# Kernel optimization log

Measured on AMD Instinct MI355X. Metric: run time of the kernel, lower is better.

The kernel has to match this reference:

```python
import jax, jax.numpy as jnp
import numpy as np

B, T, H, W = 512, 8, 28, 28
VTH, VRESET = 1.0, 0.0
ALPHA = 2.0  # spikingjelly ATan surrogate default alpha


@jax.custom_vjp
def heaviside_atan(x):
    # forward: binary spike; backward: ATan surrogate gradient
    return (x >= 0).astype(x.dtype)

def _ha_fwd(x):
    return (x >= 0).astype(x.dtype), x

def _ha_bwd(x, g):
    return (g * (ALPHA / 2.0) / (1.0 + (jnp.pi / 2.0 * ALPHA * x) ** 2),)

heaviside_atan.defvjp(_ha_fwd, _ha_bwd)


def conv3x3(x, w):
    return jax.lax.conv_general_dilated(
        x, w, (1, 1), 'SAME', dimension_numbers=('NCHW', 'OIHW', 'NCHW'))


def maxpool2(x):
    return jax.lax.reduce_window(x, -jnp.inf, jax.lax.max,
                                 (1, 1, 2, 2), (1, 1, 2, 2), 'VALID')


def one_spike_if(v, fired, x):
    # OneSpikeIFNode: integrate, fire at most once (fired mask), hard reset
    v = v + x
    spike = heaviside_atan(v - VTH) * (1.0 - fired)
    v = v * (1.0 - spike) + VRESET * spike
    fired = jnp.maximum(fired, jax.lax.stop_gradient(spike))
    return v, fired, spike


def if_node(v, x):
    # readout IFNode: integrate, fire, hard reset (v_threshold finite: latency mode, no warmup)
    v = v + x
    spike = heaviside_atan(v - VTH)
    v = v * (1.0 - spike) + VRESET * spike
    return v, spike


def setup_inputs() -> dict:
    key = jax.random.key(0)
    k = jax.random.split(key, 5)
    x = jax.random.uniform(k[0], (B, 1, H, W), jnp.float32)
    # weight scale (default_T / T) == 1 since T == 8 == default_T
    w_sconv = jax.random.normal(k[1], (16, 1, 3, 3), jnp.float32) * (2.0 / 3.0)
    w_conv = jax.random.normal(k[2], (16, 16, 3, 3), jnp.float32) * 0.12
    w_fc1 = jax.random.normal(k[3], (100, 16 * 14 * 14), jnp.float32) * 0.02
    w_fc2 = jax.random.normal(k[4], (10, 100), jnp.float32) * 0.15
    return {"x": x, "w_sconv": w_sconv, "w_conv": w_conv, "w_fc1": w_fc1, "w_fc2": w_fc2}


def reference(x, w_sconv, w_conv, w_fc1, w_fc2):
    xs = conv3x3(x, w_sconv)  # static conv computed once, reused every timestep
    z = jnp.zeros_like(xs)                       # [B,16,28,28]
    zp = jnp.zeros((B, 16, 14, 14), xs.dtype)    # pool fired-window mask
    zf = jnp.zeros((B, 100), xs.dtype)
    zo = jnp.zeros((B, 10), xs.dtype)
    state0 = (z, z, z, z, zp, zf, zf, zo)

    def step(state, _):
        v1, f1, v2, f2, pf, vfc, ffc, vout = state
        v1, f1, s1 = one_spike_if(v1, f1, xs)
        c = conv3x3(s1, w_conv)
        v2, f2, s2 = one_spike_if(v2, f2, c)
        # FirstSpikePool2d: max-pool spikes, each window passes only its first spike
        pooled = maxpool2(s2) * (1.0 - pf)
        pf = jnp.maximum(pf, jax.lax.stop_gradient(pooled))
        h = pooled.reshape(B, -1) @ w_fc1.T      # [B,100]
        vfc, ffc, s3 = one_spike_if(vfc, ffc, h)
        o = s3 @ w_fc2.T                          # [B,10]
        vout, s4 = if_node(vout, o)
        fr = jnp.stack([s1.mean(), s2.mean(), s3.mean(), s4.mean()])
        return (v1, f1, v2, f2, pf, vfc, ffc, vout), (s4, vout, fr)

    _, (s4_t, vout_t, fr_t) = jax.lax.scan(step, state0, None, length=T)
    counter_t = jnp.cumsum(s4_t, axis=0)                        # [T,B,10]
    latency_score = heaviside_atan(counter_t - 0.5).sum(axis=0)  # ATan_binary surrogate
    reg_loss = fr_t.max(axis=0).sum()
    return latency_score / T, reg_loss
```

## Files before the change

### kernel.cpp

```cpp
#include <hip/hip_runtime.h>

#define TB 1024
#define NIMG 512
#define HW 28
#define NPIX 784
#define TT 8
#define NFC 100
#define NOUT 10
#define MAGIC 0x5C5C5C5Cu

#define WT_FLOATS 313600
#define GLB_ADD(p, v) __hip_atomic_fetch_add((p), (v), __ATOMIC_RELAXED, __HIP_MEMORY_SCOPE_AGENT)

typedef float f4 __attribute__((ext_vector_type(4)));

__device__ __forceinline__ void wave_sum4(unsigned int& a, unsigned int& b,
                                          unsigned int& c, unsigned int& d) {
#pragma unroll
    for (int s = 1; s < 64; s <<= 1) {
        a += __shfl_xor(a, s);
        b += __shfl_xor(b, s);
        c += __shfl_xor(c, s);
        d += __shfl_xor(d, s);
    }
}

__global__ __launch_bounds__(TB, 8)
void snn_main(const float* __restrict__ xg, const float* __restrict__ w_sconv,
              const float* __restrict__ w_conv, const float* __restrict__ w_fc1,
              const float* __restrict__ w_fc2, float* __restrict__ wT,
              float* __restrict__ out, unsigned int* __restrict__ ctrl)
{
    __shared__ float wc[2880];
    __shared__ unsigned char spanB[25600];
    __shared__ unsigned short rowOr[TT * HW];
    __shared__ unsigned char tqA[3136];
    __shared__ unsigned short slist[3136];
    __shared__ float xst[NPIX];
    __shared__ float wsc[144];
    __shared__ int bcnt[9], bofs[9], bput[8];
    __shared__ int hist[32];
    __shared__ int lastflag;

    unsigned short* mask_t = (unsigned short*)spanB;
    unsigned int* mask32 = (unsigned int*)spanB;
    unsigned int* t2n = (unsigned int*)(spanB + 12544);
    float* prefixLDS = (float*)spanB;

    unsigned int* tflags = ctrl;
    float* fr_g = (float*)(ctrl + 98);
    unsigned int* done2 = ctrl + 130;
    unsigned int* fr_ready = ctrl + 131;

    const int tid = threadIdx.x;
    const int b = blockIdx.x;
    const int lane = tid & 63;

    if (b < 98) {
        const int c0 = b * 32;
        for (int idx = tid; idx < 3200; idx += TB) {
            int c = idx / 100, r = idx - 100 * c;
            wT[(c0 + c) * 100 + r] = w_fc1[r * 3136 + c0 + c];
        }
    }
    if (b == 0 && tid < 33) ctrl[98 + tid] = 0u;

    for (int i = tid; i < NPIX; i += TB) xst[i] = xg[b * NPIX + i];
    for (int i = tid; i < 144; i += TB) wsc[i] = w_sconv[i];
    for (int i = tid; i < 2304; i += TB) {
        int c = i & 15, r = i >> 4;
        wc[r * 20 + c] = w_conv[c * 144 + r];
    }
    for (int i = tid; i < 3136; i += TB) mask32[i] = 0u;
    if (tid < 32) hist[tid] = 0;
    if (tid < 9) bcnt[tid] = 0;
    if (b < 98) __threadfence();
    __syncthreads();
    if (b < 98 && tid == 0) {
        __hip_atomic_store(&tflags[b], MAGIC, __ATOMIC_RELEASE, __HIP_MEMORY_SCOPE_AGENT);
        if (b == 0)
            __hip_atomic_store(fr_ready, MAGIC, __ATOMIC_RELEASE, __HIP_MEMORY_SCOPE_AGENT);
    }

    unsigned int pca = 0, pcb = 0;
#pragma unroll 1
    for (int e = 0; e < 13; e++) {
        int g = e * TB + tid;
        if (g < 12544) {
            int ci = g & 15, pos = g >> 4;
            int yy = pos / HW, xx = pos % HW;
            float acc = 0.f;
#pragma unroll
            for (int ky = 0; ky < 3; ky++) {
                int ys = yy + ky - 1;
                if (ys < 0 || ys >= HW) continue;
#pragma unroll
                for (int kx = 0; kx < 3; kx++) {
                    int xsrc = xx + kx - 1;
                    if (xsrc < 0 || xsrc >= HW) continue;
                    acc = fmaf(wsc[ci * 9 + ky * 3 + kx], xst[ys * HW + xsrc], acc);
                }
            }
            int t1 = 8; float v = 0.f;
#pragma unroll
            for (int t = 0; t < TT; t++) {
                v += acc;
                if (t1 == 8 && v >= 1.0f) t1 = t;
            }
            if (t1 < 8) {
                int lin = t1 * NPIX + pos;
                atomicOr(&mask32[lin >> 1], (1u << ci) << ((lin & 1) * 16));
                if (t1 < 4) pca += 1u << (t1 * 8); else pcb += 1u << ((t1 - 4) * 8);
            }
        }
    }
    {
        unsigned int a_lo = pca & 0x00ff00ffu, a_hi = (pca >> 8) & 0x00ff00ffu;
        unsigned int b_lo = pcb & 0x00ff00ffu, b_hi = (pcb >> 8) & 0x00ff00ffu;
        wave_sum4(a_lo, a_hi, b_lo, b_hi);
        if (lane == 0) {
            if (a_lo & 0xffffu)  atomicAdd(&hist[0], (int)(a_lo & 0xffffu));
            if (a_hi & 0xffffu)  atomicAdd(&hist[1], (int)(a_hi & 0xffffu));
            if (a_lo >> 16)      atomicAdd(&hist[2], (int)(a_lo >> 16));
            if (a_hi >> 16)      atomicAdd(&hist[3], (int)(a_hi >> 16));
            if (b_lo & 0xffffu)  atomicAdd(&hist[4], (int)(b_lo & 0xffffu));
            if (b_hi & 0xffffu)  atomicAdd(&hist[5], (int)(b_hi & 0xffffu));
            if (b_lo >> 16)      atomicAdd(&hist[6], (int)(b_lo >> 16));
            if (b_hi >> 16)      atomicAdd(&hist[7], (int)(b_hi >> 16));
        }
    }
    __syncthreads();

    for (int i = tid; i < TT * HW; i += TB) {
        const unsigned short* mr = mask_t + (i / HW) * NPIX + (i % HW) * HW;
        unsigned int o = 0;
#pragma unroll
        for (int x = 0; x < HW; x++) o |= mr[x];
        rowOr[i] = (unsigned short)o;
    }
    __syncthreads();

    unsigned int pc2a = 0, pc2b = 0;
    {
        int run = tid >> 4;
        int pos = (run < 49) ? ((run * 18) % 49) * 16 + (tid & 15) : -1;
        if (pos >= 0) {
            int py = pos / HW, px = pos - py * HW;
            f4 vv0 = {0.f, 0.f, 0.f, 0.f}, vv1 = vv0, vv2 = vv0, vv3 = vv0;
            unsigned int done = 0;
            unsigned int t2lo = 0x88888888u, t2hi = 0x88888888u;
#pragma unroll 1
            for (int t = 0; t < TT; t++) {
                const unsigned short* ro = rowOr + t * HW;
                unsigned int un = ro[py];
                if (py > 0) un |= ro[py - 1];
                if (py < HW - 1) un |= ro[py + 1];
                if (!un) continue;
                const unsigned short* mt = mask_t + t * NPIX;
#pragma unroll
                for (int k = 0; k < 9; k++) {
                    int qy = py + k / 3 - 1, qx = px + k % 3 - 1;
                    if ((unsigned)qy >= HW || (unsigned)qx >= HW) continue;
                    unsigned int m = mt[qy * HW + qx];
                    while (m) {
                        int ci = __builtin_ctz(m); m &= m - 1;
                        const f4* wrow = (const f4*)&wc[(ci * 9 + k) * 20];
                        vv0 += wrow[0]; vv1 += wrow[1];
                        vv2 += wrow[2]; vv3 += wrow[3];
                    }
                }
                unsigned int fired = 0;
#pragma unroll
                for (int c = 0; c < 16; c++) {
                    float val = (c < 4) ? vv0[c & 3] : (c < 8) ? vv1[c & 3]
                              : (c < 12) ? vv2[c & 3] : vv3[c & 3];
                    fired |= (val >= 1.0f) ? (1u << c) : 0u;
                }
                unsigned int newf = fired & ~done;
                done |= newf;
                if (newf) {
                    int cnt = __builtin_popcount(newf);
                    if (t < 4) pc2a += (unsigned)cnt << (t * 8);
                    else       pc2b += (unsigned)cnt << ((t - 4) * 8);
                    while (newf) {
                        int c = __builtin_ctz(newf); newf &= newf - 1;
                        if (c < 8) t2lo = (t2lo & ~(15u << (4 * c))) | ((unsigned)t << (4 * c));
                        else       t2hi = (t2hi & ~(15u << (4 * (c - 8)))) | ((unsigned)t << (4 * (c - 8)));
                    }
                }
                if (done == 0xffffu) break;
            }
            t2n[pos * 2] = t2lo;
            t2n[pos * 2 + 1] = t2hi;
        }
    }
    {
        unsigned int a_lo = pc2a & 0x00ff00ffu, a_hi = (pc2a >> 8) & 0x00ff00ffu;
        unsigned int b_lo = pc2b & 0x00ff00ffu, b_hi = (pc2b >> 8) & 0x00ff00ffu;
        wave_sum4(a_lo, a_hi, b_lo, b_hi);
        if (lane == 0) {
            if (a_lo & 0xffffu)  atomicAdd(&hist[8],  (int)(a_lo & 0xffffu));
            if (a_hi & 0xffffu)  atomicAdd(&hist[9],  (int)(a_hi & 0xffffu));
            if (a_lo >> 16)      atomicAdd(&hist[10], (int)(a_lo >> 16));
            if (a_hi >> 16)      atomicAdd(&hist[11], (int)(a_hi >> 16));
            if (b_lo & 0xffffu)  atomicAdd(&hist[12], (int)(b_lo & 0xffffu));
            if (b_hi & 0xffffu)  atomicAdd(&hist[13], (int)(b_hi & 0xffffu));
            if (b_lo >> 16)      atomicAdd(&hist[14], (int)(b_lo >> 16));
            if (b_hi >> 16)      atomicAdd(&hist[15], (int)(b_hi >> 16));
        }
    }
    __syncthreads();

    {
        unsigned int cpa = 0, cpb = 0;
        for (int u = tid; u < 3136; u += TB) {
            int c = u / 196, rem = u - c * 196;
            int wy = rem / 14, wx = rem - wy * 14;
            int p0 = wy * 56 + wx * 2;
            int wsel = c >> 3, sh = (c & 7) * 4;
            int m0 = (t2n[p0 * 2 + wsel] >> sh) & 15;
            int m1 = (t2n[(p0 + 1) * 2 + wsel] >> sh) & 15;
            int m2 = (t2n[(p0 + HW) * 2 + wsel] >> sh) & 15;
            int m3 = (t2n[(p0 + HW + 1) * 2 + wsel] >> sh) & 15;
            int tqv = min(min(m0, m1), min(m2, m3));
            tqA[u] = (unsigned char)tqv;
            if (tqv < 8) {
                if (tqv < 4) cpa += 1u << (tqv * 8);
                else         cpb += 1u << ((tqv - 4) * 8);
            }
        }
        unsigned int a_lo = cpa & 0x00ff00ffu, a_hi = (cpa >> 8) & 0x00ff00ffu;
        unsigned int b_lo = cpb & 0x00ff00ffu, b_hi = (cpb >> 8) & 0x00ff00ffu;
        wave_sum4(a_lo, a_hi, b_lo, b_hi);
        if (lane == 0) {
            if (a_lo & 0xffffu)  atomicAdd(&bcnt[0], (int)(a_lo & 0xffffu));
            if (a_hi & 0xffffu)  atomicAdd(&bcnt[1], (int)(a_hi & 0xffffu));
            if (a_lo >> 16)      atomicAdd(&bcnt[2], (int)(a_lo >> 16));
            if (a_hi >> 16)      atomicAdd(&bcnt[3], (int)(a_hi >> 16));
            if (b_lo & 0xffffu)  atomicAdd(&bcnt[4], (int)(b_lo & 0xffffu));
            if (b_hi & 0xffffu)  atomicAdd(&bcnt[5], (int)(b_hi & 0xffffu));
            if (b_lo >> 16)      atomicAdd(&bcnt[6], (int)(b_lo >> 16));
            if (b_hi >> 16)      atomicAdd(&bcnt[7], (int)(b_hi >> 16));
        }
    }
    __syncthreads();
    if (tid == 0) {
        int s = 0;
#pragma unroll
        for (int t = 0; t < TT; t++) { bofs[t] = s; s += bcnt[t]; }
        bofs[8] = s;
    }
    __syncthreads();
    if (tid < 8) bput[tid] = bofs[tid];
    __syncthreads();
    for (int base_u = 0; base_u < 3136; base_u += TB) {
        int u = base_u + tid;
        int tqv = (u < 3136) ? (int)tqA[u] : 8;
#pragma unroll 1
        for (int v = 0; v < TT; v++) {
            unsigned long long m = __ballot(tqv == v);
            if (!m) continue;
            int lead = __ffsll((unsigned long long)m) - 1;
            int bs = 0;
            if (lane == lead) bs = atomicAdd(&bput[v], __popcll(m));
            bs = __shfl(bs, lead);
            if (tqv == v) {
                int rank = __popcll(m & ((1ull << lane) - 1ull));
                slist[bs + rank] = (unsigned short)u;
            }
        }
    }

    if (tid < 98) {
        while (__hip_atomic_load(&tflags[tid], __ATOMIC_ACQUIRE,
                                 __HIP_MEMORY_SCOPE_AGENT) != MAGIC)
            __builtin_amdgcn_s_sleep(2);
    }
    __syncthreads();

    {
        const int w = tid >> 7;
        const int sub = (tid >> 6) & 1;
        const int col = sub * 64 + lane;
        const bool act = col < NFC;
        const float* wA = wT + col;
        float acc0 = 0.f;
#pragma unroll 1
        for (int t = 0; t < TT; t++) {
            const int lo = bofs[t];
            const int n = bofs[t + 1] - lo;
            int j = w;
            for (; j + 56 < n; j += 64) {
                int u0 = (int)slist[lo + j] * 100;
                int u1 = (int)slist[lo + j + 8] * 100;
                int u2 = (int)slist[lo + j + 16] * 100;
                int u3 = (int)slist[lo + j + 24] * 100;
                int u4 = (int)slist[lo + j + 32] * 100;
                int u5 = (int)slist[lo + j + 40] * 100;
                int u6 = (int)slist[lo + j + 48] * 100;
                int u7 = (int)slist[lo + j + 56] * 100;
                if (act) {
                    float a0 = wA[u0], a1 = wA[u1], a2 = wA[u2], a3 = wA[u3];
                    float a4 = wA[u4], a5 = wA[u5], a6 = wA[u6], a7 = wA[u7];
                    acc0 += a0; acc0 += a1; acc0 += a2; acc0 += a3;
                    acc0 += a4; acc0 += a5; acc0 += a6; acc0 += a7;
                }
            }
            for (; j + 24 < n; j += 32) {
                int u0 = (int)slist[lo + j] * 100;
                int u1 = (int)slist[lo + j + 8] * 100;
                int u2 = (int)slist[lo + j + 16] * 100;
                int u3 = (int)slist[lo + j + 24] * 100;
                if (act) {
                    float a0 = wA[u0], a1 = wA[u1], a2 = wA[u2], a3 = wA[u3];
                    acc0 += a0; acc0 += a1; acc0 += a2; acc0 += a3;
                }
            }
            for (; j < n; j += 8) {
                int u0 = (int)slist[lo + j] * 100;
                if (act) acc0 += wA[u0];
            }
            if (act) prefixLDS[(w * TT + t) * NFC + col] = acc0;
        }
    }
    __syncthreads();

    if (tid < NFC) {
        int t3 = 8;
#pragma unroll
        for (int t = 0; t < TT; t++) {
            float v = 0.f;
#pragma unroll
            for (int w = 0; w < 8; w++) v += prefixLDS[(w * TT + t) * NFC + tid];
            if (t3 == 8 && v >= 1.0f) t3 = t;
        }
        tqA[tid] = (unsigned char)t3;
        if (t3 < 8) atomicAdd(&hist[16 + t3], 1);
    }
    __syncthreads();

    if (tid < 640) {
        const int o = tid >> 6;
        float acc8[TT] = {0.f, 0.f, 0.f, 0.f, 0.f, 0.f, 0.f, 0.f};
        {
            float wv = w_fc2[o * NFC + lane];
            int tv = tqA[lane];
#pragma unroll
            for (int k = 0; k < TT; k++) acc8[k] += (tv == k) ? wv : 0.f;
        }
        if (lane < 36) {
            float wv = w_fc2[o * NFC + 64 + lane];
            int tv = tqA[64 + lane];
#pragma unroll
            for (int k = 0; k < TT; k++) acc8[k] += (tv == k) ? wv : 0.f;
        }
#pragma unroll
        for (int s = 1; s < 64; s <<= 1) {
#pragma unroll
            for (int k = 0; k < TT; k++) acc8[k] += __shfl_xor(acc8[k], s);
        }
        if (lane == 0) {
            float vout = 0.f; int cnt = 0; float lat = 0.f;
#pragma unroll
            for (int t = 0; t < TT; t++) {
                vout += acc8[t];
                if (vout >= 1.0f) { vout = 0.f; cnt++; atomicAdd(&hist[24 + t], 1); }
                if (cnt >= 1) lat += 1.f;
            }
            out[b * NOUT + o] = lat * 0.125f;
        }
    }
    __syncthreads();

    if (tid == 0) {
        while (__hip_atomic_load(fr_ready, __ATOMIC_ACQUIRE,
                                 __HIP_MEMORY_SCOPE_AGENT) != MAGIC)
            __builtin_amdgcn_s_sleep(2);
    }
    __syncthreads();
    if (tid < 32) {
        int h = hist[tid];
        if (h) GLB_ADD(&fr_g[(tid & 7) * 4 + (tid >> 3)], (float)h);
    }
    __syncthreads();

    if (tid == 0) {
        unsigned int old = __hip_atomic_fetch_add(done2, 1u, __ATOMIC_ACQ_REL,
                                                  __HIP_MEMORY_SCOPE_AGENT);
        lastflag = (old == (unsigned)(NIMG - 1));
    }
    __syncthreads();
    if (lastflag && tid == 0) {
        const float inv0 = 1.f / 6422528.f;
        const float inv2 = 1.f / 51200.f;
        const float inv3 = 1.f / 5120.f;
        const float invs[4] = { inv0, inv0, inv2, inv3 };
        float reg = 0.f;
        for (int l = 0; l < 4; l++) {
            float mx = -INFINITY;
            for (int t = 0; t < TT; t++) {
                float v = __hip_atomic_load(&fr_g[t * 4 + l], __ATOMIC_RELAXED,
                                            __HIP_MEMORY_SCOPE_AGENT);
                mx = fmaxf(mx, v * invs[l]);
            }
            reg += mx;
        }
        out[NIMG * NOUT] = reg;
    }
}

extern "C" void kernel_launch(void* const* d_in, const int* in_sizes, int n_in,
                              void* d_out, int out_size, void* d_ws, size_t ws_size,
                              hipStream_t stream) {
    const float* x       = (const float*)d_in[0];
    const float* w_sconv = (const float*)d_in[1];
    const float* w_conv  = (const float*)d_in[2];
    const float* w_fc1   = (const float*)d_in[3];
    const float* w_fc2   = (const float*)d_in[4];
    float* out = (float*)d_out;

    float* wT          = (float*)d_ws;
    unsigned int* ctrl = (unsigned int*)(wT + WT_FLOATS);

    snn_main<<<NIMG, TB, 0, stream>>>(x, w_sconv, w_conv, w_fc1, w_fc2, wT,
                                      out, ctrl);
}
```

Before: 173.5 us.

## Pad spike mask planes and sort conv2 pixels by neighbor spike load

Stores the layer-1 first-spike masks in zero-padded 30x30 planes, so the conv2 gather reads nine neighbor masks without bounds checks. It packs them into five words and walks the set bits in one combined loop. It also counts layer-1 spikes per pixel and bucket-sorts the 784 output pixels by their 3x3 neighborhood spike count, so lanes in a wave get similar amounts of work and diverge less. This replaces the rowOr skip test and the fixed permutation, at the cost of extra ballot/atomic sorting passes and more shared memory.

```diff
diff --git a/kernel.cpp b/kernel.cpp
--- a/kernel.cpp
+++ b/kernel.cpp
@@ -4,6 +4,8 @@
 #define NIMG 512
 #define HW 28
 #define NPIX 784
+#define PW 30
+#define PPLANE 900
 #define TT 8
 #define NFC 100
 #define NOUT 10
@@ -33,19 +35,22 @@
 {
     __shared__ float wc[2880];
     __shared__ unsigned char spanB[25600];
-    __shared__ unsigned short rowOr[TT * HW];
-    __shared__ unsigned char tqA[3136];
+    __shared__ int tqAi[784];
     __shared__ unsigned short slist[3136];
     __shared__ float xst[NPIX];
     __shared__ float wsc[144];
     __shared__ int bcnt[9], bofs[9], bput[8];
+    __shared__ int s32cnt[32], s32ofs[33], s32put[32];
     __shared__ int hist[32];
     __shared__ int lastflag;
 
-    unsigned short* mask_t = (unsigned short*)spanB;
-    unsigned int* mask32 = (unsigned int*)spanB;
-    unsigned int* t2n = (unsigned int*)(spanB + 12544);
+    unsigned short* maskP = (unsigned short*)spanB;
+    unsigned int* maskP32 = (unsigned int*)spanB;
+    unsigned int* t2n = (unsigned int*)(spanB + 14400);
     float* prefixLDS = (float*)spanB;
+    unsigned char* tqA = (unsigned char*)tqAi;
+    unsigned char* cntA = (unsigned char*)tqAi;
+    unsigned short* sorted2 = slist;
 
     unsigned int* tflags = ctrl;
     float* fr_g = (float*)(ctrl + 98);
@@ -71,8 +76,9 @@
         int c = i & 15, r = i >> 4;
         wc[r * 20 + c] = w_conv[c * 144 + r];
     }
-    for (int i = tid; i < 3136; i += TB) mask32[i] = 0u;
-    if (tid < 32) hist[tid] = 0;
+    for (int i = tid; i < 3600; i += TB) maskP32[i] = 0u;
+    if (tid < 225) tqAi[tid] = 0;
+    if (tid < 32) { hist[tid] = 0; s32cnt[tid] = 0; }
     if (tid < 9) bcnt[tid] = 0;
     if (b < 98) __threadfence();
     __syncthreads();
@@ -86,9 +92,11 @@
 #pragma unroll 1
     for (int e = 0; e < 13; e++) {
         int g = e * TB + tid;
+        int t1 = 8;
+        int yy = 0, xx = 0;
         if (g < 12544) {
             int ci = g & 15, pos = g >> 4;
-            int yy = pos / HW, xx = pos % HW;
+            yy = pos / HW; xx = pos - yy * HW;
             float acc = 0.f;
 #pragma unroll
             for (int ky = 0; ky < 3; ky++) {
@@ -101,17 +109,22 @@
                     acc = fmaf(wsc[ci * 9 + ky * 3 + kx], xst[ys * HW + xsrc], acc);
                 }
             }
-            int t1 = 8; float v = 0.f;
+            float v = 0.f;
 #pragma unroll
             for (int t = 0; t < TT; t++) {
                 v += acc;
                 if (t1 == 8 && v >= 1.0f) t1 = t;
             }
             if (t1 < 8) {
-                int lin = t1 * NPIX + pos;
-                atomicOr(&mask32[lin >> 1], (1u << ci) << ((lin & 1) * 16));
+                int lin = t1 * PPLANE + (yy + 1) * PW + (xx + 1);
+                atomicOr(&maskP32[lin >> 1], (1u << ci) << ((lin & 1) * 16));
                 if (t1 < 4) pca += 1u << (t1 * 8); else pcb += 1u << ((t1 - 4) * 8);
             }
+        }
+        unsigned long long bal = __ballot(g < 12544 && t1 < 8);
+        if (g < 12544 && (tid & 15) == 0) {
+            int cnt = (int)__popcll((bal >> (lane & 48)) & 0xFFFFull);
+            cntA[(yy + 1) * PW + (xx + 1)] = (unsigned char)cnt;
         }
     }
     {
@@ -131,40 +144,70 @@
     }
     __syncthreads();
 
-    for (int i = tid; i < TT * HW; i += TB) {
-        const unsigned short* mr = mask_t + (i / HW) * NPIX + (i % HW) * HW;
-        unsigned int o = 0;
-#pragma unroll
-        for (int x = 0; x < HW; x++) o |= mr[x];
-        rowOr[i] = (unsigned short)o;
+    int myb = 32;
+    if (tid < NPIX) {
+        int py = tid / HW, px = tid - py * HW;
+        const unsigned char* cb = cntA + py * PW + px;
+        int nb = cb[0] + cb[1] + cb[2] + cb[PW] + cb[PW + 1] + cb[PW + 2]
+               + cb[2 * PW] + cb[2 * PW + 1] + cb[2 * PW + 2];
+        myb = min(nb >> 2, 31);
+    }
+#pragma unroll 1
+    for (int v = 0; v < 32; v++) {
+        unsigned long long mm = __ballot(myb == v);
+        if (mm && lane == 0) atomicAdd(&s32cnt[v], (int)__popcll(mm));
+    }
+    __syncthreads();
+    if (tid == 0) {
+        int s = 0;
+#pragma unroll 1
+        for (int v = 0; v < 32; v++) { s32ofs[v] = s; s += s32cnt[v]; }
+        s32ofs[32] = s;
+    }
+    __syncthreads();
+    if (tid < 32) s32put[tid] = s32ofs[tid];
+    __syncthreads();
+#pragma unroll 1
+    for (int v = 0; v < 32; v++) {
+        unsigned long long mm = __ballot(myb == v);
+        if (!mm) continue;
+        int lead = __ffsll(mm) - 1;
+        int bs = 0;
+        if (lane == lead) bs = atomicAdd(&s32put[v], (int)__popcll(mm));
+        bs = __shfl(bs, lead);
+        if (myb == v) {
+            int rank = (int)__popcll(mm & ((1ull << lane) - 1ull));
+            sorted2[bs + rank] = (unsigned short)tid;
+        }
     }
     __syncthreads();
 
     unsigned int pc2a = 0, pc2b = 0;
     {
-        int run = tid >> 4;
-        int pos = (run < 49) ? ((run * 18) % 49) * 16 + (tid & 15) : -1;
+        const int pos = (tid < NPIX) ? (int)sorted2[tid] : -1;
         if (pos >= 0) {
-            int py = pos / HW, px = pos - py * HW;
+            const int py = pos / HW, px = pos - py * HW;
+            const unsigned short* mbase = maskP + py * PW + px;
             f4 vv0 = {0.f, 0.f, 0.f, 0.f}, vv1 = vv0, vv2 = vv0, vv3 = vv0;
             unsigned int done = 0;
             unsigned int t2lo = 0x88888888u, t2hi = 0x88888888u;
 #pragma unroll 1
             for (int t = 0; t < TT; t++) {
-                const unsigned short* ro = rowOr + t * HW;
-                unsigned int un = ro[py];
-                if (py > 0) un |= ro[py - 1];
-                if (py < HW - 1) un |= ro[py + 1];
-                if (!un) continue;
-                const unsigned short* mt = mask_t + t * NPIX;
-#pragma unroll
-                for (int k = 0; k < 9; k++) {
-                    int qy = py + k / 3 - 1, qx = px + k % 3 - 1;
-                    if ((unsigned)qy >= HW || (unsigned)qx >= HW) continue;
-                    unsigned int m = mt[qy * HW + qx];
-                    while (m) {
-                        int ci = __builtin_ctz(m); m &= m - 1;
-                        const f4* wrow = (const f4*)&wc[(ci * 9 + k) * 20];
+                const unsigned short* mt = mbase + t * PPLANE;
+                unsigned int Mw0 = (unsigned)mt[0]          | ((unsigned)mt[1] << 16);
+                unsigned int Mw1 = (unsigned)mt[2]          | ((unsigned)mt[PW] << 16);
+                unsigned int Mw2 = (unsigned)mt[PW + 1]     | ((unsigned)mt[PW + 2] << 16);
+                unsigned int Mw3 = (unsigned)mt[2 * PW]     | ((unsigned)mt[2 * PW + 1] << 16);
+                unsigned int Mw4 = (unsigned)mt[2 * PW + 2];
+                if (!(Mw0 | Mw1 | Mw2 | Mw3 | Mw4)) continue;
+                unsigned int Mw[5] = {Mw0, Mw1, Mw2, Mw3, Mw4};
+#pragma unroll
+                for (int w = 0; w < 5; w++) {
+                    unsigned int M = Mw[w];
+                    while (M) {
+                        int bit = __builtin_ctz(M); M &= M - 1;
+                        int row = (bit & 15) * 9 + w * 2 + (bit >> 4);
+                        const f4* wrow = (const f4*)&wc[row * 20];
                         vv0 += wrow[0]; vv1 += wrow[1];
                         vv2 += wrow[2]; vv3 += wrow[3];
                     }
```

New measurement: 183.4 us. 5.7% more time.
